# Kernel tuning notes

Measured on AMD Instinct MI355X. Metric: run time of the kernel, lower is better.

The kernel has to match this reference:

```python
import jax, jax.numpy as jnp
import numpy as np

B, R, S, NI, C, HW, HID = 4, 4096, 48, 48, 32, 256, 64

PLANE_AXES = np.array([[[1, 0, 0], [0, 1, 0], [0, 0, 1]],
                       [[0, 0, 1], [1, 0, 0], [0, 1, 0]],
                       [[0, 1, 0], [0, 0, 1], [1, 0, 0]]], dtype=np.float32)
INV_PLANES = jnp.asarray(np.linalg.inv(PLANE_AXES))  # [3,3,3]


def setup_inputs():
    key = jax.random.key(0)
    ks = jax.random.split(key, 6)
    planes = 0.1 * jax.random.normal(ks[0], (B, 3, C, HW, HW), jnp.float32)
    ray_origins = jnp.array([0., 0., 2.7], jnp.float32) + 0.05 * jax.random.normal(ks[1], (B, R, 3), jnp.float32)
    d = 0.15 * jax.random.normal(ks[2], (B, R, 3), jnp.float32) + jnp.array([0., 0., -1.], jnp.float32)
    ray_directions = d / jnp.linalg.norm(d, axis=-1, keepdims=True)
    w1 = jax.random.normal(ks[3], (C, HID), jnp.float32) / np.sqrt(C).astype(np.float32)
    b1 = jnp.zeros((HID,), jnp.float32)
    w2 = jax.random.normal(ks[4], (HID, 4), jnp.float32) / np.sqrt(HID).astype(np.float32)
    b2 = jnp.zeros((4,), jnp.float32)
    return dict(planes=planes, ray_origins=ray_origins, ray_directions=ray_directions,
                w1=w1, b1=b1, w2=w2, b2=b2)


def _grid_sample_bilinear(img, coords):
    # img [C,H,W], coords [M,2] (x,y) in [-1,1]; zeros padding, align_corners=False
    Ch, H, W = img.shape
    x = (coords[:, 0] + 1.) * 0.5 * W - 0.5
    y = (coords[:, 1] + 1.) * 0.5 * H - 0.5
    x0 = jnp.floor(x)
    y0 = jnp.floor(y)
    wx = x - x0
    wy = y - y0

    def tap(xi, yi, w):
        valid = (xi >= 0) & (xi < W) & (yi >= 0) & (yi < H)
        xi_ = jnp.clip(xi, 0, W - 1).astype(jnp.int32)
        yi_ = jnp.clip(yi, 0, H - 1).astype(jnp.int32)
        return img[:, yi_, xi_] * (w * valid)[None, :]

    out = (tap(x0, y0, (1 - wx) * (1 - wy)) + tap(x0 + 1, y0, wx * (1 - wy))
           + tap(x0, y0 + 1, (1 - wx) * wy) + tap(x0 + 1, y0 + 1, wx * wy))
    return out.T  # [M,C]


def sample_from_planes(planes, coords):
    # planes [B,3,C,H,W], coords [B,M,3] -> features [B,3,M,C]
    Bn, P, Ch, H, W = planes.shape
    proj = jnp.einsum('bmi,pij->bpmj', coords, INV_PLANES)[..., :2]  # project_onto_planes
    out = jax.vmap(_grid_sample_bilinear)(planes.reshape(Bn * P, Ch, H, W),
                                          proj.reshape(Bn * P, -1, 2))
    return out.reshape(Bn, P, -1, Ch)


def decoder_mlp(feat, w1, b1, w2, b2):
    # OSGDecoder-style: mean over tri-planes, 2-layer MLP -> (sdf, rgb)
    x = feat.mean(axis=1)  # [B,M,C]
    h = jax.nn.softplus(x @ w1 + b1)
    o = h @ w2 + b2
    sdf = o[..., :1]
    rgb = jax.nn.sigmoid(o[..., 1:]) * 1.002 - 0.001
    sigma = 10.0 * jax.nn.softplus(-10.0 * sdf)  # sdf2sigma (VolSDF-style)
    return rgb, sigma


def ray_march(colors, densities, depths):
    # MipRayMarcher2: midpoint compositing along the sample axis
    deltas = depths[:, :, 1:] - depths[:, :, :-1]
    cm = 0.5 * (colors[:, :, :-1] + colors[:, :, 1:])
    dm = 0.5 * (densities[:, :, :-1] + densities[:, :, 1:])
    zm = 0.5 * (depths[:, :, :-1] + depths[:, :, 1:])
    alpha = 1.0 - jnp.exp(-deltas * dm)
    trans = jnp.cumprod(jnp.concatenate([jnp.ones_like(alpha[:, :, :1]),
                                         1.0 - alpha + 1e-10], axis=2), axis=2)[:, :, :-1]
    weights = alpha * trans
    return (weights * cm).sum(2), (weights * zm).sum(2), weights


def sample_pdf(bins, weights, n_imp, eps=1e-5):
    # inverse-CDF sampling (deterministic u), searchsorted + gather
    w = weights + eps
    cdf = jnp.cumsum(w / w.sum(-1, keepdims=True), -1)
    cdf = jnp.concatenate([jnp.zeros_like(cdf[:, :1]), cdf], -1)
    u = jnp.broadcast_to(jnp.linspace(0., 1., n_imp), (bins.shape[0], n_imp))
    inds = jax.vmap(lambda c, uu: jnp.searchsorted(c, uu, side='right'))(cdf, u)
    below = jnp.maximum(inds - 1, 0)
    above = jnp.minimum(inds, weights.shape[1])
    cdf_b = jnp.take_along_axis(cdf, below, 1)
    cdf_a = jnp.take_along_axis(cdf, above, 1)
    bin_b = jnp.take_along_axis(bins, below, 1)
    bin_a = jnp.take_along_axis(bins, above, 1)
    denom = jnp.where(cdf_a - cdf_b < eps, 1.0, cdf_a - cdf_b)
    return bin_b + (u - cdf_b) / denom * (bin_a - bin_b)


def sample_importance(depths, weights, n_imp):
    Bn, Rn = depths.shape[:2]
    w = weights.reshape(Bn * Rn, -1)
    wp = jnp.pad(w, ((0, 0), (1, 1)))
    wm = jnp.maximum(wp[:, :-1], wp[:, 1:])      # max_pool1d(k=2,s=1,p=1)
    w = 0.5 * (wm[:, :-1] + wm[:, 1:]) + 0.01    # avg_pool1d(k=2,s=1) + 0.01
    z_mid = 0.5 * (depths[:, :, :-1, 0] + depths[:, :, 1:, 0]).reshape(Bn * Rn, -1)
    z = sample_pdf(z_mid, w[:, 1:-1], n_imp)
    return jax.lax.stop_gradient(z).reshape(Bn, Rn, n_imp, 1)


def _forward(planes, ray_origins, ray_directions, w1, b1, w2, b2):
    # dda near/far from camera distance (fallback branch of dda())
    cam = jnp.linalg.norm(ray_origins, axis=-1, keepdims=True)  # [B,R,1]
    near, far = cam - 0.5, cam + 0.5
    t = (jnp.arange(S, dtype=jnp.float32) + 0.5) / S  # stratified midpoints (deterministic)
    depths = near[:, :, None, :] + (far - near)[:, :, None, :] * t[None, None, :, None]

    def run(dz):
        sp = dz.shape[2]
        coords = (ray_origins[:, :, None, :] + dz * ray_directions[:, :, None, :]).reshape(B, -1, 3)
        rgb, sigma = decoder_mlp(sample_from_planes(planes, coords), w1, b1, w2, b2)
        return rgb.reshape(B, R, sp, 3), sigma.reshape(B, R, sp, 1)

    colors_c, dens_c = run(depths)
    _, _, weights = ray_march(colors_c, dens_c, depths)
    depths_f = sample_importance(depths, weights, NI)
    colors_f, dens_f = run(depths_f)

    # unify_samples: concat + sort by depth + gather
    d = jnp.concatenate([depths, depths_f], 2)
    c = jnp.concatenate([colors_c, colors_f], 2)
    s = jnp.concatenate([dens_c, dens_f], 2)
    idx = jnp.argsort(d, axis=2)
    d = jnp.take_along_axis(d, idx, 2)
    c = jnp.take_along_axis(c, idx, 2)
    s = jnp.take_along_axis(s, idx, 2)
    rgb_final, depth_final, w = ray_march(c, s, d)
    return rgb_final, depth_final, w.sum(2)


def reference(planes, ray_origins, ray_directions, w1, b1, w2, b2):
    return _forward(planes, ray_origins, ray_directions, w1, b1, w2, b2)
```

## Files before the change

kernel.cpp:

```cpp
#include <hip/hip_runtime.h>
#include <hip/hip_fp16.h>
#include <math.h>

#define NB 4
#define NR 4096
#define NS 48
#define PLANE_ELEMS (65536*32)

typedef _Float16 f16x8 __attribute__((ext_vector_type(8)));
typedef float    f32x4 __attribute__((ext_vector_type(4)));

__device__ __forceinline__ float coarse_depth(float cam, int i) {
    float nearv = cam - 0.5f;
    float farv  = cam + 0.5f;
    float t = ((float)i + 0.5f) / 48.0f;
    return nearv + (farv - nearv) * t;
}
__device__ __forceinline__ float softplusf(float x) {
    return fmaxf(x, 0.0f) + __logf(1.0f + __expf(-fabsf(x)));
}
__device__ __forceinline__ float sigmoidf(float x) {
    return 1.0f / (1.0f + __expf(-x));
}

__global__ __launch_bounds__(256) void k_transpose(const float* __restrict__ src,
                                                   __half* __restrict__ dst,
                                                   const float* __restrict__ w1,
                                                   unsigned* __restrict__ w1frag) {
    if (blockIdx.x == 3072) {
        int t = threadIdx.x;
        for (int f = t; f < 1024; f += 256) {
            int ht = f >> 8, rem = f & 255, lane = rem >> 2, qq = rem & 3;
            int quad = lane >> 4, m = lane & 15;
            int k0 = quad*8 + 2*qq;
            __half lo = __float2half_rn(w1[(k0+0)*64 + ht*16 + m]);
            __half hi = __float2half_rn(w1[(k0+1)*64 + ht*16 + m]);
            w1frag[f] = (unsigned)__half_as_ushort(lo)
                      | ((unsigned)__half_as_ushort(hi) << 16);
        }
        return;
    }
    __shared__ unsigned short tile[256*33];
    int bp = blockIdx.x >> 8;
    int y  = blockIdx.x & 255;
    int t  = threadIdx.x;
    const float* s = src + (size_t)bp*PLANE_ELEMS + (size_t)y*256;
    #pragma unroll
    for (int c = 0; c < 32; ++c)
        tile[t*33 + c] = __half_as_ushort(__float2half_rn(s[(size_t)c*65536 + t]));
    __syncthreads();
    unsigned* d = reinterpret_cast<unsigned*>(dst + ((size_t)bp*65536 + (size_t)y*256)*32);
    #pragma unroll
    for (int it = 0; it < 16; ++it) {
        int q = it*256 + t;
        int x = q >> 4, c2 = q & 15;
        unsigned lo = tile[x*33 + 2*c2];
        unsigned hi = tile[x*33 + 2*c2 + 1];
        d[q] = lo | (hi << 16);
    }
}

__global__ __launch_bounds__(256, 5) void k_sample_mlp(
    const __half* __restrict__ planesT,
    const float* __restrict__ orig, const float* __restrict__ dirs,
    const unsigned* __restrict__ w1frag, const float* __restrict__ b1,
    const float* __restrict__ w2, const float* __restrict__ b2,
    const float* __restrict__ dfine,
    float* __restrict__ colors, float* __restrict__ sigmas,
    int mode)
{
    __shared__ unsigned desc[256*12];
    __shared__ unsigned featT[256*16];
    __shared__ float b1s[64];
    __shared__ float w2s[256];

    int tid = threadIdx.x;
    int pid = blockIdx.x * 256 + tid;
    int rid = pid / 48;
    int s   = pid - rid*48;
    int b   = rid >> 12;

    float ox = orig[rid*3+0], oy = orig[rid*3+1], oz = orig[rid*3+2];
    float dxv = dirs[rid*3+0], dyv = dirs[rid*3+1], dzv = dirs[rid*3+2];
    float depth;
    if (mode == 0) {
        float cam = sqrtf(ox*ox + oy*oy + oz*oz);
        depth = coarse_depth(cam, s);
    } else {
        depth = dfine[(size_t)rid*48 + s];
    }
    float cx = ox + depth*dxv;
    float cy = oy + depth*dyv;
    float cz = oz + depth*dzv;
    float us[3] = {cx, cz, cy};
    float vs[3] = {cy, cx, cz};
    unsigned dpk[12];
    #pragma unroll
    for (int pl = 0; pl < 3; ++pl) {
        float xg = (us[pl] + 1.0f) * 0.5f * 256.0f - 0.5f;
        float yg = (vs[pl] + 1.0f) * 0.5f * 256.0f - 0.5f;
        float x0f = floorf(xg), y0f = floorf(yg);
        float wx = xg - x0f, wy = yg - y0f;
        int x0 = (int)x0f, y0 = (int)y0f;
        float tw[4] = {(1.0f-wx)*(1.0f-wy), wx*(1.0f-wy), (1.0f-wx)*wy, wx*wy};
        #pragma unroll
        for (int t4 = 0; t4 < 4; ++t4) {
            int xi = x0 + (t4 & 1);
            int yi = y0 + (t4 >> 1);
            bool valid = (xi >= 0) && (xi < 256) && (yi >= 0) && (yi < 256);
            int xc = min(max(xi, 0), 255);
            int yc = min(max(yi, 0), 255);
            float wv = valid ? tw[t4] : 0.0f;
            dpk[pl*4+t4] = ((unsigned)__half_as_ushort(__float2half_rn(wv)) << 16)
                         | (unsigned)(yc*256 + xc);
        }
    }
    #pragma unroll
    for (int q = 0; q < 6; ++q)
        *reinterpret_cast<uint2*>(&desc[tid*12 + 2*q]) = make_uint2(dpk[2*q], dpk[2*q+1]);
    if (tid < 64) {
        b1s[tid] = b1[tid];
        *reinterpret_cast<float4*>(&w2s[tid*4]) =
            *reinterpret_cast<const float4*>(&w2[tid*4]);
    }
    __syncthreads();

    int lane = tid & 63, wbase = tid & 192;
    int g8 = lane >> 3, sub = lane & 7, c0 = sub*4;
    const __half* pbase = planesT + (size_t)(b*3)*PLANE_ELEMS + c0;
    const __half2 inv3h = __float2half2_rn(1.0f/3.0f);
    #pragma unroll 2
    for (int it = 0; it < 8; ++it) {
        int pp = wbase + it*8 + g8;
        __half2 a01 = __float2half2_rn(0.0f);
        __half2 a23 = __float2half2_rn(0.0f);
        #pragma unroll
        for (int h6 = 0; h6 < 2; ++h6) {
            unsigned dd[6];
            #pragma unroll
            for (int q = 0; q < 3; ++q) {
                uint2 pr = *reinterpret_cast<const uint2*>(&desc[pp*12 + h6*6 + 2*q]);
                dd[2*q] = pr.x; dd[2*q+1] = pr.y;
            }
            uint2 v[6]; __half2 wv[6];
            #pragma unroll
            for (int q = 0; q < 6; ++q) {
                int tp = h6*6 + q;
                int tix = dd[q] & 0xFFFF;
                wv[q] = __half2half2(__ushort_as_half((unsigned short)(dd[q] >> 16)));
                v[q] = *reinterpret_cast<const uint2*>(
                    pbase + (size_t)(tp>>2)*PLANE_ELEMS + ((size_t)tix << 5));
            }
            #pragma unroll
            for (int q = 0; q < 6; ++q) {
                __half2 v01, v23;
                __builtin_memcpy(&v01, &v[q].x, 4);
                __builtin_memcpy(&v23, &v[q].y, 4);
                a01 = __hfma2(wv[q], v01, a01);
                a23 = __hfma2(wv[q], v23, a23);
            }
        }
        a01 = __hmul2(a01, inv3h);
        a23 = __hmul2(a23, inv3h);
        unsigned u01, u23;
        __builtin_memcpy(&u01, &a01, 4);
        __builtin_memcpy(&u23, &a23, 4);
        int base = pp*16 + (((sub>>1) ^ (pp&3)) << 2) + ((sub&1) << 1);
        *reinterpret_cast<uint2*>(&featT[base]) = make_uint2(u01, u23);
    }
    asm volatile("s_waitcnt lgkmcnt(0)" ::: "memory");

    int w    = tid >> 6;
    int quad = lane >> 4;
    int n    = lane & 15;
    f16x8 af[4];
    {
        const uint4* wf = reinterpret_cast<const uint4*>(w1frag);
        #pragma unroll
        for (int ht = 0; ht < 4; ++ht) {
            uint4 u = wf[ht*64 + lane];
            __builtin_memcpy(&af[ht], &u, 16);
        }
    }
    #pragma unroll
    for (int p = 0; p < 4; ++p) {
        int ptile = w*4 + p;
        int pt    = ptile*16 + n;
        uint4 bu = *reinterpret_cast<const uint4*>(
            &featT[pt*16 + ((quad ^ (pt&3)) << 2)]);
        f16x8 bf;
        __builtin_memcpy(&bf, &bu, 16);
        float o0=0.f, o1=0.f, o2=0.f, o3=0.f;
        #pragma unroll
        for (int ht = 0; ht < 4; ++ht) {
            f32x4 acc = {0.f, 0.f, 0.f, 0.f};
            acc = __builtin_amdgcn_mfma_f32_16x16x32_f16(af[ht], bf, acc, 0, 0, 0);
            float4 bb = *reinterpret_cast<const float4*>(&b1s[ht*16 + quad*4]);
            float bbv[4] = {bb.x, bb.y, bb.z, bb.w};
            #pragma unroll
            for (int r = 0; r < 4; ++r) {
                float hv = softplusf(acc[r] + bbv[r]);
                float4 wr = *reinterpret_cast<const float4*>(
                    &w2s[(ht*16 + quad*4 + r)*4]);
                o0 = fmaf(hv, wr.x, o0);
                o1 = fmaf(hv, wr.y, o1);
                o2 = fmaf(hv, wr.z, o2);
                o3 = fmaf(hv, wr.w, o3);
            }
        }
        o0 += __shfl_xor(o0, 16); o0 += __shfl_xor(o0, 32);
        o1 += __shfl_xor(o1, 16); o1 += __shfl_xor(o1, 32);
        o2 += __shfl_xor(o2, 16); o2 += __shfl_xor(o2, 32);
        o3 += __shfl_xor(o3, 16); o3 += __shfl_xor(o3, 32);
        int pid2 = blockIdx.x*256 + ptile*16 + n;
        int rid2 = pid2 / 48;
        int s2   = pid2 - rid2*48;
        int slot = rid2*96 + (mode ? 48 + s2 : s2);
        if (quad == 0) {
            sigmas[slot] = 10.0f * softplusf(-10.0f * (o0 + b2[0]));
        } else {
            float oc = (quad == 1) ? o1 : (quad == 2 ? o2 : o3);
            colors[(size_t)slot*3 + (quad-1)] =
                sigmoidf(oc + b2[quad]) * 1.002f - 0.001f;
        }
    }
}

__global__ __launch_bounds__(64) void k_importance(
    const float* __restrict__ orig, const float* __restrict__ sigmas,
    float* __restrict__ dfine)
{
    __shared__ float tile[64*49];
    int t  = threadIdx.x;
    int r0 = blockIdx.x * 64;
    for (int it = 0; it < 48; ++it) {
        int l  = it*64 + t;
        int ri = l / 48;
        int i  = l - ri*48;
        tile[ri*49 + i] = sigmas[(size_t)(r0+ri)*96 + i];
    }
    __syncthreads();
    int rid = r0 + t;
    float ox = orig[rid*3+0], oy = orig[rid*3+1], oz = orig[rid*3+2];
    float cam = sqrtf(ox*ox + oy*oy + oz*oz);

    float w[47];
    float T = 1.0f;
    float sp_ = tile[t*49 + 0];
    float dprev = coarse_depth(cam, 0);
    #pragma unroll
    for (int i = 0; i < 47; ++i) {
        float sc = tile[t*49 + i + 1];
        float dnext = coarse_depth(cam, i+1);
        float delta = dnext - dprev;
        float dm = 0.5f*(sp_ + sc);
        float a = 1.0f - __expf(-delta*dm);
        w[i] = a * T;
        T *= (1.0f - a + 1e-10f);
        sp_ = sc; dprev = dnext;
    }
    float Ssum = 0.0f;
    #pragma unroll
    for (int m = 0; m < 45; ++m) {
        float wm1 = fmaxf(w[m],   w[m+1]);
        float wm2 = fmaxf(w[m+1], w[m+2]);
        float wq = (0.5f*(wm1 + wm2) + 0.01f) + 1e-5f;
        tile[t*49 + m] = wq;
        Ssum += wq;
    }
    int idx = 1;
    float cprev = 0.0f;
    float ccur  = tile[t*49 + 0] / Ssum;
    for (int k = 0; k < 48; ++k) {
        float u = (float)k * (1.0f/47.0f);
        while (idx < 46 && ccur <= u) {
            cprev = ccur;
            idx++;
            if (idx < 46) ccur += tile[t*49 + (idx-1)] / Ssum;
        }
        int below = idx - 1;
        int above = min(idx, 45);
        float cb = cprev;
        float ca = (idx < 46) ? ccur : cprev;
        float bb = 0.5f*(coarse_depth(cam, below) + coarse_depth(cam, below+1));
        float ba = 0.5f*(coarse_depth(cam, above) + coarse_depth(cam, above+1));
        float d_ = ca - cb;
        float den = (d_ < 1e-5f) ? 1.0f : d_;
        dfine[(size_t)rid*48 + k] = bb + (u - cb)/den * (ba - bb);
    }
}

__global__ __launch_bounds__(64) void k_final(
    const float* __restrict__ orig,
    const float* __restrict__ colors, const float* __restrict__ sigmas,
    const float* __restrict__ dfine, float* __restrict__ out)
{
    __shared__ float scol[32*289];
    __shared__ float ssig[32*97];
    __shared__ float sdf [32*49];
    int t  = threadIdx.x;
    int r0 = blockIdx.x * 32;

    {
        const float4* src = reinterpret_cast<const float4*>(colors + (size_t)r0*288);
        for (int q = t; q < 2304; q += 64) {
            float4 v = src[q];
            int e = q*4, row = e/288, col = e - row*288;
            scol[row*289+col+0] = v.x; scol[row*289+col+1] = v.y;
            scol[row*289+col+2] = v.z; scol[row*289+col+3] = v.w;
        }
    }
    {
        const float4* src = reinterpret_cast<const float4*>(sigmas + (size_t)r0*96);
        for (int q = t; q < 768; q += 64) {
            float4 v = src[q];
            int e = q*4, row = e/96, col = e - row*96;
            ssig[row*97+col+0] = v.x; ssig[row*97+col+1] = v.y;
            ssig[row*97+col+2] = v.z; ssig[row*97+col+3] = v.w;
        }
    }
    {
        const float4* src = reinterpret_cast<const float4*>(dfine + (size_t)r0*48);
        for (int q = t; q < 384; q += 64) {
            float4 v = src[q];
            int e = q*4, row = e/48, col = e - row*48;
            sdf[row*49+col+0] = v.x; sdf[row*49+col+1] = v.y;
            sdf[row*49+col+2] = v.z; sdf[row*49+col+3] = v.w;
        }
    }
    __syncthreads();
    if (t >= 32) return;

    int rid = r0 + t;
    float ox = orig[rid*3+0], oy = orig[rid*3+1], oz = orig[rid*3+2];
    float cam = sqrtf(ox*ox + oy*oy + oz*oz);
    int i = 0, j = 0;
    float T = 1.0f, rgb0=0.f, rgb1=0.f, rgb2=0.f, dep=0.f, wsum=0.f;
    float dprev=0.f, sprev=0.f, cp0=0.f, cp1=0.f, cp2=0.f;
    for (int m = 0; m < 96; ++m) {
        float dc = (i < 48) ? coarse_depth(cam, i) : 3.4e38f;
        float df = (j < 48) ? sdf[t*49 + j] : 3.4e38f;
        bool takec = dc <= df;
        int slot = takec ? i : 48 + j;
        float dcur = takec ? dc : df;
        if (takec) ++i; else ++j;
        float sc = ssig[t*97 + slot];
        float c0 = scol[t*289 + slot*3+0];
        float c1 = scol[t*289 + slot*3+1];
        float c2 = scol[t*289 + slot*3+2];
        if (m > 0) {
            float delta = dcur - dprev;
            float dm = 0.5f*(sprev + sc);
            float zm = 0.5f*(dprev + dcur);
            float a = 1.0f - __expf(-delta*dm);
            float wgt = a * T;
            T *= (1.0f - a + 1e-10f);
            rgb0 += wgt*0.5f*(cp0 + c0);
            rgb1 += wgt*0.5f*(cp1 + c1);
            rgb2 += wgt*0.5f*(cp2 + c2);
            dep  += wgt*zm;
            wsum += wgt;
        }
        dprev = dcur; sprev = sc; cp0 = c0; cp1 = c1; cp2 = c2;
    }
    out[rid*3+0] = rgb0;
    out[rid*3+1] = rgb1;
    out[rid*3+2] = rgb2;
    out[16384*3 + rid] = dep;
    out[16384*4 + rid] = wsum;
}

extern "C" void kernel_launch(void* const* d_in, const int* in_sizes, int n_in,
                              void* d_out, int out_size, void* d_ws, size_t ws_size,
                              hipStream_t stream)
{
    const float* planes = (const float*)d_in[0];
    const float* orig   = (const float*)d_in[1];
    const float* dirs   = (const float*)d_in[2];
    const float* w1     = (const float*)d_in[3];
    const float* b1     = (const float*)d_in[4];
    const float* w2     = (const float*)d_in[5];
    const float* b2     = (const float*)d_in[6];
    float* out = (float*)d_out;

    float* ws = (float*)d_ws;
    size_t n_sig = (size_t)NB*NR*96;
    size_t n_col = n_sig*3;
    size_t n_df  = (size_t)NB*NR*48;
    float*  sig     = ws;
    float*  col     = sig + n_sig;
    float*  dfin    = col + n_col;
    __half* planesT = (__half*)(dfin + n_df);
    unsigned* w1frag = (unsigned*)(planesT + (size_t)12*PLANE_ELEMS);

    k_transpose<<<3073, 256, 0, stream>>>(planes, planesT, w1, w1frag);
    k_sample_mlp<<<3072, 256, 0, stream>>>(planesT, orig, dirs,
                                           w1frag, b1, w2, b2, dfin, col, sig, 0);
    k_importance<<<256, 64, 0, stream>>>(orig, sig, dfin);
    k_sample_mlp<<<3072, 256, 0, stream>>>(planesT, orig, dirs,
                                           w1frag, b1, w2, b2, dfin, col, sig, 1);
    k_final<<<512, 64, 0, stream>>>(orig, col, sig, dfin, out);
}
```

Baseline: 337.8 us.

## Shuffle compact sample descriptors instead of LDS table, vectorize plane transpose

The plane transpose kernel now reads float4 rows and packs channel pairs before writing uint4 outputs through a padded 32-bit LDS tile, replacing scalar 16-bit traffic. The sample kernel drops the 12-entry per-point descriptor array in LDS. It packs one base offset plus dx/dy flags and two half2 weight words per plane, and broadcasts them with wave shuffles, deriving the four tap addresses arithmetically. It also raises the occupancy hint to 8 waves per SIMD and folds the b1 bias into the MFMA accumulator init. The aim is less LDS traffic and register pressure, at the cost of extra shuffles and tighter register limits.

```diff
diff --git a/kernel.cpp b/kernel.cpp
--- a/kernel.cpp
+++ b/kernel.cpp
@@ -40,27 +40,45 @@
         }
         return;
     }
-    __shared__ unsigned short tile[256*33];
+    __shared__ unsigned tile32[16*260];
     int bp = blockIdx.x >> 8;
     int y  = blockIdx.x & 255;
     int t  = threadIdx.x;
-    const float* s = src + (size_t)bp*PLANE_ELEMS + (size_t)y*256;
-    #pragma unroll
-    for (int c = 0; c < 32; ++c)
-        tile[t*33 + c] = __half_as_ushort(__float2half_rn(s[(size_t)c*65536 + t]));
+    const float4* s4 = reinterpret_cast<const float4*>(
+        src + (size_t)bp*PLANE_ELEMS + (size_t)y*256);
+    #pragma unroll
+    for (int it = 0; it < 4; ++it) {
+        int idx = it*256 + t;
+        int cp = idx >> 6, x4 = idx & 63;
+        float4 a = s4[(size_t)(2*cp)*16384 + x4];
+        float4 b = s4[(size_t)(2*cp+1)*16384 + x4];
+        unsigned u0 = (unsigned)__half_as_ushort(__float2half_rn(a.x))
+                    | ((unsigned)__half_as_ushort(__float2half_rn(b.x)) << 16);
+        unsigned u1 = (unsigned)__half_as_ushort(__float2half_rn(a.y))
+                    | ((unsigned)__half_as_ushort(__float2half_rn(b.y)) << 16);
+        unsigned u2 = (unsigned)__half_as_ushort(__float2half_rn(a.z))
+                    | ((unsigned)__half_as_ushort(__float2half_rn(b.z)) << 16);
+        unsigned u3 = (unsigned)__half_as_ushort(__float2half_rn(a.w))
+                    | ((unsigned)__half_as_ushort(__float2half_rn(b.w)) << 16);
+        *reinterpret_cast<uint4*>(&tile32[cp*260 + x4*4]) = make_uint4(u0,u1,u2,u3);
+    }
     __syncthreads();
-    unsigned* d = reinterpret_cast<unsigned*>(dst + ((size_t)bp*65536 + (size_t)y*256)*32);
-    #pragma unroll
-    for (int it = 0; it < 16; ++it) {
-        int q = it*256 + t;
-        int x = q >> 4, c2 = q & 15;
-        unsigned lo = tile[x*33 + 2*c2];
-        unsigned hi = tile[x*33 + 2*c2 + 1];
-        d[q] = lo | (hi << 16);
-    }
-}
-
-__global__ __launch_bounds__(256, 5) void k_sample_mlp(
+    uint4* d4 = reinterpret_cast<uint4*>(
+        reinterpret_cast<unsigned*>(dst + ((size_t)bp*65536 + (size_t)y*256)*32));
+    #pragma unroll
+    for (int it = 0; it < 4; ++it) {
+        int v = it*256 + t;
+        int x = v >> 2, cq = v & 3;
+        uint4 val;
+        val.x = tile32[(cq*4+0)*260 + x];
+        val.y = tile32[(cq*4+1)*260 + x];
+        val.z = tile32[(cq*4+2)*260 + x];
+        val.w = tile32[(cq*4+3)*260 + x];
+        d4[v] = val;
+    }
+}
+
+__global__ __launch_bounds__(256, 8) void k_sample_mlp(
     const __half* __restrict__ planesT,
     const float* __restrict__ orig, const float* __restrict__ dirs,
     const unsigned* __restrict__ w1frag, const float* __restrict__ b1,
@@ -69,7 +87,6 @@
     float* __restrict__ colors, float* __restrict__ sigmas,
     int mode)
 {
-    __shared__ unsigned desc[256*12];
     __shared__ unsigned featT[256*16];
     __shared__ float b1s[64];
     __shared__ float w2s[256];
@@ -94,7 +111,7 @@
     float cz = oz + depth*dzv;
     float us[3] = {cx, cz, cy};
     float vs[3] = {cy, cx, cz};
-    unsigned dpk[12];
+    unsigned opk[3], wpk[6];
     #pragma unroll
     for (int pl = 0; pl < 3; ++pl) {
         float xg = (us[pl] + 1.0f) * 0.5f * 256.0f - 0.5f;
@@ -102,22 +119,24 @@
         float x0f = floorf(xg), y0f = floorf(yg);
         float wx = xg - x0f, wy = yg - y0f;
         int x0 = (int)x0f, y0 = (int)y0f;
-        float tw[4] = {(1.0f-wx)*(1.0f-wy), wx*(1.0f-wy), (1.0f-wx)*wy, wx*wy};
-        #pragma unroll
-        for (int t4 = 0; t4 < 4; ++t4) {
-            int xi = x0 + (t4 & 1);
-            int yi = y0 + (t4 >> 1);
-            bool valid = (xi >= 0) && (xi < 256) && (yi >= 0) && (yi < 256);
-            int xc = min(max(xi, 0), 255);
-            int yc = min(max(yi, 0), 255);
-            float wv = valid ? tw[t4] : 0.0f;
-            dpk[pl*4+t4] = ((unsigned)__half_as_ushort(__float2half_rn(wv)) << 16)
-                         | (unsigned)(yc*256 + xc);
-        }
-    }
-    #pragma unroll
-    for (int q = 0; q < 6; ++q)
-        *reinterpret_cast<uint2*>(&desc[tid*12 + 2*q]) = make_uint2(dpk[2*q], dpk[2*q+1]);
+        int xc0 = min(max(x0,   0), 255), yc0 = min(max(y0,   0), 255);
+        int xc1 = min(max(x0+1, 0), 255), yc1 = min(max(y0+1, 0), 255);
+        bool bx0 = (x0 >= 0)  && (x0 < 256);
+        bool bx1 = (x0 >= -1) && (x0 <= 254);
+        bool by0 = (y0 >= 0)  && (y0 < 256);
+        bool by1 = (y0 >= -1) && (y0 <= 254);
+        float w00 = (bx0 && by0) ? (1.0f-wx)*(1.0f-wy) : 0.0f;
+        float w10 = (bx1 && by0) ? wx*(1.0f-wy)        : 0.0f;
+        float w01 = (bx0 && by1) ? (1.0f-wx)*wy        : 0.0f;
+        float w11 = (bx1 && by1) ? wx*wy               : 0.0f;
+        opk[pl] = (unsigned)(pl*65536 + yc0*256 + xc0)
+                | ((unsigned)(xc1 - xc0) << 18)
+                | ((unsigned)(yc1 - yc0) << 19);
+        wpk[2*pl+0] = (unsigned)__half_as_ushort(__float2half_rn(w00))
+                    | ((unsigned)__half_as_ushort(__float2half_rn(w10)) << 16);
+        wpk[2*pl+1] = (unsigned)__half_as_ushort(__float2half_rn(w01))
+                    | ((unsigned)__half_as_ushort(__float2half_rn(w11)) << 16);
+    }
     if (tid < 64) {
         b1s[tid] = b1[tid];
         *reinterpret_cast<float4*>(&w2s[tid*4]) =
@@ -126,47 +145,61 @@
     __syncthreads();
 
     int lane = tid & 63, wbase = tid & 192;
-    int g8 = lane >> 3, sub = lane & 7, c0 = sub*4;
-    const __half* pbase = planesT + (size_t)(b*3)*PLANE_ELEMS + c0;
+    int g8 = lane >> 3, sub = lane & 7;
+    unsigned c02 = (unsigned)(sub * 8);
+    const char* pb = reinterpret_cast<const char*>(planesT)
+                   + (size_t)(b*3) * (size_t)PLANE_ELEMS * 2;
     const __half2 inv3h = __float2half2_rn(1.0f/3.0f);
     #pragma unroll 2
     for (int it = 0; it < 8; ++it) {
-        int pp = wbase + it*8 + g8;
+        int pp   = wbase + it*8 + g8;
+        int srcl = it*8 + g8;
+        unsigned ov0 = __shfl(opk[0], srcl, 64);
+        unsigned ov1 = __shfl(opk[1], srcl, 64);
+        unsigned ov2 = __shfl(opk[2], srcl, 64);
+        unsigned wv2[6];
+        #pragma unroll
+        for (int q = 0; q < 6; ++q) wv2[q] = __shfl(wpk[q], srcl, 64);
+        unsigned ov[3] = {ov0, ov1, ov2};
         __half2 a01 = __float2half2_rn(0.0f);
         __half2 a23 = __float2half2_rn(0.0f);
         #pragma unroll
-        for (int h6 = 0; h6 < 2; ++h6) {
-            unsigned dd[6];
-            #pragma unroll
-            for (int q = 0; q < 3; ++q) {
-                uint2 pr = *reinterpret_cast<const uint2*>(&desc[pp*12 + h6*6 + 2*q]);
-                dd[2*q] = pr.x; dd[2*q+1] = pr.y;
-            }
-            uint2 v[6]; __half2 wv[6];
-            #pragma unroll
-            for (int q = 0; q < 6; ++q) {
-                int tp = h6*6 + q;
-                int tix = dd[q] & 0xFFFF;
-                wv[q] = __half2half2(__ushort_as_half((unsigned short)(dd[q] >> 16)));
-                v[q] = *reinterpret_cast<const uint2*>(
-                    pbase + (size_t)(tp>>2)*PLANE_ELEMS + ((size_t)tix << 5));
-            }
-            #pragma unroll
-            for (int q = 0; q < 6; ++q) {
-                __half2 v01, v23;
-                __builtin_memcpy(&v01, &v[q].x, 4);
-                __builtin_memcpy(&v23, &v[q].y, 4);
-                a01 = __hfma2(wv[q], v01, a01);
-                a23 = __hfma2(wv[q], v23, a23);
-            }
+        for (int pl = 0; pl < 3; ++pl) {
+            unsigned v    = ov[pl];
+            unsigned base = ((v & 0x3FFFFu) << 6) + c02;
+            unsigned dxb  = (v >> 12) & 64u;
+            unsigned dyb  = (v >> 5)  & 16384u;
+            uint2 t0 = *reinterpret_cast<const uint2*>(pb + base);
+            uint2 t1 = *reinterpret_cast<const uint2*>(pb + (base + dxb));
+            uint2 t2 = *reinterpret_cast<const uint2*>(pb + (base + dyb));
+            uint2 t3 = *reinterpret_cast<const uint2*>(pb + (base + dxb + dyb));
+            unsigned wl = wv2[2*pl], wh = wv2[2*pl+1];
+            unsigned uw00 = __builtin_amdgcn_perm(wl, wl, 0x01000100u);
+            unsigned uw10 = __builtin_amdgcn_perm(wl, wl, 0x03020302u);
+            unsigned uw01 = __builtin_amdgcn_perm(wh, wh, 0x01000100u);
+            unsigned uw11 = __builtin_amdgcn_perm(wh, wh, 0x03020302u);
+            __half2 w00h, w10h, w01h, w11h;
+            __builtin_memcpy(&w00h, &uw00, 4);
+            __builtin_memcpy(&w10h, &uw10, 4);
+            __builtin_memcpy(&w01h, &uw01, 4);
+            __builtin_memcpy(&w11h, &uw11, 4);
+            __half2 v01, v23;
+            __builtin_memcpy(&v01, &t0.x, 4); __builtin_memcpy(&v23, &t0.y, 4);
+            a01 = __hfma2(w00h, v01, a01);    a23 = __hfma2(w00h, v23, a23);
+            __builtin_memcpy(&v01, &t1.x, 4); __builtin_memcpy(&v23, &t1.y, 4);
+            a01 = __hfma2(w10h, v01, a01);    a23 = __hfma2(w10h, v23, a23);
+            __builtin_memcpy(&v01, &t2.x, 4); __builtin_memcpy(&v23, &t2.y, 4);
+            a01 = __hfma2(w01h, v01, a01);    a23 = __hfma2(w01h, v23, a23);
+            __builtin_memcpy(&v01, &t3.x, 4); __builtin_memcpy(&v23, &t3.y, 4);
+            a01 = __hfma2(w11h, v01, a01);    a23 = __hfma2(w11h, v23, a23);
         }
         a01 = __hmul2(a01, inv3h);
         a23 = __hmul2(a23, inv3h);
         unsigned u01, u23;
         __builtin_memcpy(&u01, &a01, 4);
         __builtin_memcpy(&u23, &a23, 4);
-        int base = pp*16 + (((sub>>1) ^ (pp&3)) << 2) + ((sub&1) << 1);
-        *reinterpret_cast<uint2*>(&featT[base]) = make_uint2(u01, u23);
+        int basew = pp*16 + (((sub>>1) ^ (pp&3)) << 2) + ((sub&1) << 1);
+        *reinterpret_cast<uint2*>(&featT[basew]) = make_uint2(u01, u23);
     }
     asm volatile("s_waitcnt lgkmcnt(0)" ::: "memory");
 
@@ -193,13 +226,12 @@
         float o0=0.f, o1=0.f, o2=0.f, o3=0.f;
         #pragma unroll
         for (int ht = 0; ht < 4; ++ht) {
-            f32x4 acc = {0.f, 0.f, 0.f, 0.f};
+            float4 bb = *reinterpret_cast<const float4*>(&b1s[ht*16 + quad*4]);
+            f32x4 acc = {bb.x, bb.y, bb.z, bb.w};
             acc = __builtin_amdgcn_mfma_f32_16x16x32_f16(af[ht], bf, acc, 0, 0, 0);
-            float4 bb = *reinterpret_cast<const float4*>(&b1s[ht*16 + quad*4]);
-            float bbv[4] = {bb.x, bb.y, bb.z, bb.w};
             #pragma unroll
             for (int r = 0; r < 4; ++r) {
-                float hv = softplusf(acc[r] + bbv[r]);
+                float hv = softplusf(acc[r]);
                 float4 wr = *reinterpret_cast<const float4*>(
                     &w2s[(ht*16 + quad*4 + r)*4]);
                 o0 = fmaf(hv, wr.x, o0);
```

Result: slower. 353.9 us (+4.8%).
